# Performance work log

Hardware: AMD Instinct MI355X
Metric: run time of the kernel (lower is better)

## Reference

```python
import jax, jax.numpy as jnp
import numpy as np
from jax import lax

FILTER_SIZE = 3
C_IN = 128
C_OUT = 256
PAD = 1
STRIDE = 1


def setup_inputs() -> dict:
    key = jax.random.key(0)
    k1, k2 = jax.random.split(key)
    prev_a = jax.random.normal(k1, (32, 56, 56, C_IN), dtype=jnp.float32)
    # filter_w initialized ~ N(0, 1) as in the original tf.random.normal
    filter_w = jax.random.normal(k2, (FILTER_SIZE, FILTER_SIZE, C_IN, C_OUT), dtype=jnp.float32)
    filter_b = jnp.zeros((1, 1, 1, C_OUT), dtype=jnp.float32)
    return {"prev_a": prev_a, "filter_w": filter_w, "filter_b": filter_b}


def reference(prev_a, filter_w, filter_b):
    # NHWC input, HWIO filter -> NHWC output; same math as the nested-loop conv:
    # z[i,h,w,c] = sum(prev_a_pad[i, h*s:h*s+f, w*s:w*s+f, :] * W[:,:,:,c]) + b[c]
    z = lax.conv_general_dilated(
        prev_a,
        filter_w,
        window_strides=(STRIDE, STRIDE),
        padding=[(PAD, PAD), (PAD, PAD)],
        dimension_numbers=("NHWC", "HWIO", "NHWC"),
    )
    z = z + filter_b  # bias broadcast over (m, H, W)
    return jax.nn.relu(z)
```

## Files before the change

kernel.cpp:

```cpp
#include <hip/hip_runtime.h>
#include <hip/hip_bf16.h>


#define NIMG 32
#define HH 56
#define WW 56
#define PH 58
#define PW 58
#define CIN 128
#define COUT 256
#define KTOT 1152
#define PAD_ELEMS (NIMG * PH * PW * CIN)

#define BK 32
#define KITERS (KTOT / BK)

typedef __attribute__((ext_vector_type(8))) short bf16x8;
typedef __attribute__((ext_vector_type(4))) short s16x4;
typedef __attribute__((ext_vector_type(4))) float f32x4;

__device__ __forceinline__ short f2bf(float x) {
    union { __hip_bfloat16 b; short s; } u;
    u.b = __float2bfloat16(x);
    return u.s;
}

typedef const void __attribute__((address_space(1)))* gas1_t;
typedef void __attribute__((address_space(3)))* las3_t;
__device__ __forceinline__ void async16(short* lds, const short* g) {
    __builtin_amdgcn_global_load_lds((gas1_t)g, (las3_t)lds, 16, 0, 0);
}

__global__ __launch_bounds__(256) void pack_input(const float* __restrict__ in,
                                                  short* __restrict__ pad) {
    const int tid  = blockIdx.x * 256 + threadIdx.x;
    const int flat = tid * 8;
    const int c8   = flat & (CIN - 1);
    const int rest = flat >> 7;
    const int iw   = rest % PW;
    const int r2   = rest / PW;
    const int ih   = r2 % PH;
    const int img  = r2 / PH;
    bf16x8 v = (bf16x8)0;
    if (ih >= 1 && ih <= HH && iw >= 1 && iw <= WW) {
        const float* p = in + (((size_t)(img * HH + ih - 1) * WW + (iw - 1)) * CIN + c8);
        const float4 x0 = *(const float4*)p;
        const float4 x1 = *(const float4*)(p + 4);
        v.s0 = f2bf(x0.x); v.s1 = f2bf(x0.y); v.s2 = f2bf(x0.z); v.s3 = f2bf(x0.w);
        v.s4 = f2bf(x1.x); v.s5 = f2bf(x1.y); v.s6 = f2bf(x1.z); v.s7 = f2bf(x1.w);
    }
    *(bf16x8*)(pad + flat) = v;
}

__global__ __launch_bounds__(256) void pack_wgt(const float* __restrict__ w,
                                                short* __restrict__ wt) {
    __shared__ short tile[32][33];
    const int k0 = blockIdx.x * 32;
    const int n0 = blockIdx.y * 32;
    const int t  = threadIdx.x;
    {
        const int kl  = t >> 3;
        const int nl4 = (t & 7) * 4;
        const float4 x = *(const float4*)(w + (size_t)(k0 + kl) * COUT + n0 + nl4);
        tile[kl][nl4 + 0] = f2bf(x.x);
        tile[kl][nl4 + 1] = f2bf(x.y);
        tile[kl][nl4 + 2] = f2bf(x.z);
        tile[kl][nl4 + 3] = f2bf(x.w);
    }
    __syncthreads();
    {
        const int nl  = t >> 3;
        const int kl4 = (t & 7) * 4;
        s16x4 v;
        v.x = tile[kl4 + 0][nl];
        v.y = tile[kl4 + 1][nl];
        v.z = tile[kl4 + 2][nl];
        v.w = tile[kl4 + 3][nl];
        *(s16x4*)(wt + (size_t)(n0 + nl) * KTOT + k0 + kl4) = v;
    }
}

__global__ __launch_bounds__(256) void conv_mfma(const short* __restrict__ apad,
                                                 const short* __restrict__ bwt,
                                                 const float* __restrict__ bias,
                                                 float* __restrict__ out) {
    __shared__ short As0[128 * BK], As1[128 * BK];
    __shared__ short Bs0[128 * BK], Bs1[128 * BK];

    const int t  = threadIdx.x;
    const int l  = t & 63;
    const int w  = t >> 6;
    const int m0 = blockIdx.y * 128;
    const int n0 = blockIdx.x * 128;

    const int Lc = (t & 7) ^ ((t >> 3) & 7);
    const int kc = Lc & 3;
    int abase[2], bbase[2];
#pragma unroll
    for (int j = 0; j < 2; ++j) {
        const int r   = 2 * (t >> 3) + (Lc >> 2) + j * 64;
        const int m   = m0 + r;
        const int img = m / (HH * WW);
        const int rem = m - img * (HH * WW);
        const int oh  = rem / WW;
        const int ow  = rem - oh * WW;
        abase[j] = ((img * PH + oh) * PW + ow) * CIN + kc * 8;
        bbase[j] = (n0 + r) * KTOT + kc * 8;
    }

    f32x4 acc[4][4];
#pragma unroll
    for (int i = 0; i < 4; ++i)
#pragma unroll
        for (int j = 0; j < 4; ++j) { f32x4 z = {0.f, 0.f, 0.f, 0.f}; acc[i][j] = z; }

    const int wm = w & 1;
    const int wn = w >> 1;
    const int fr = l & 15;
    const int fq = l >> 4;

#define STAGE(KT, AS, BS) do {                                              \
        const int _fhw  = (KT) >> 2;                                        \
        const int _fh   = _fhw / 3;                                         \
        const int _fw   = _fhw - _fh * 3;                                   \
        const int _aoff = (_fh * PW + _fw) * CIN + ((KT) & 3) * 32;         \
        const int _boff = (KT) * BK;                                        \
        _Pragma("unroll")                                                   \
        for (int _j = 0; _j < 2; ++_j) {                                    \
            async16((AS) + (_j * 256 + w * 64) * 8, apad + abase[_j] + _aoff); \
            async16((BS) + (_j * 256 + w * 64) * 8, bwt + bbase[_j] + _boff); \
        }                                                                   \
    } while (0)

#define FRAG(BASE, R) \
    (*(const bf16x8*)((BASE) + (((R) >> 1) << 6) + \
     (((((R) & 1) << 2) | fq) ^ (((R) >> 1) & 7)) * 8))

#define COMPUTE(AS, BS) do {                                                \
        bf16x8 _af[4], _bf[4];                                              \
        _Pragma("unroll")                                                   \
        for (int _i = 0; _i < 4; ++_i) _af[_i] = FRAG(AS, wm * 64 + _i * 16 + fr); \
        _Pragma("unroll")                                                   \
        for (int _j = 0; _j < 4; ++_j) _bf[_j] = FRAG(BS, wn * 64 + _j * 16 + fr); \
        _Pragma("unroll")                                                   \
        for (int _i = 0; _i < 4; ++_i)                                      \
            _Pragma("unroll")                                               \
            for (int _j = 0; _j < 4; ++_j)                                  \
                acc[_i][_j] = __builtin_amdgcn_mfma_f32_16x16x32_bf16(      \
                    _af[_i], _bf[_j], acc[_i][_j], 0, 0, 0);                \
    } while (0)

    STAGE(0, As0, Bs0);
    for (int kt = 0; kt < KITERS; kt += 2) {
        __syncthreads();
        STAGE(kt + 1, As1, Bs1);
        COMPUTE(As0, Bs0);
        __syncthreads();
        if (kt + 2 < KITERS) STAGE(kt + 2, As0, Bs0);
        COMPUTE(As1, Bs1);
    }

#pragma unroll
    for (int j = 0; j < 4; ++j) {
        const int n  = n0 + wn * 64 + j * 16 + fr;
        const float bj = bias[n];
#pragma unroll
        for (int i = 0; i < 4; ++i) {
            const int mrow = m0 + wm * 64 + i * 16 + fq * 4;
#pragma unroll
            for (int r = 0; r < 4; ++r) {
                const float v = acc[i][j][r] + bj;
                out[(size_t)(mrow + r) * COUT + n] = v > 0.f ? v : 0.f;
            }
        }
    }
#undef STAGE
#undef FRAG
#undef COMPUTE
}

extern "C" void kernel_launch(void* const* d_in, const int* in_sizes, int n_in,
                              void* d_out, int out_size, void* d_ws, size_t ws_size,
                              hipStream_t stream) {
    const float* in   = (const float*)d_in[0];
    const float* wgt  = (const float*)d_in[1];
    const float* bias = (const float*)d_in[2];
    float* out = (float*)d_out;

    short* pad = (short*)d_ws;
    short* wt  = (short*)d_ws + PAD_ELEMS;

    pack_input<<<PAD_ELEMS / 8 / 256, 256, 0, stream>>>(in, pad);
    pack_wgt<<<dim3(KTOT / 32, COUT / 32), 256, 0, stream>>>(wgt, wt);

    dim3 grid(COUT / 128, (NIMG * HH * WW) / 128);
    conv_mfma<<<grid, 256, 0, stream>>>(pad, wt, bias, out);
}
```

Before: 223.2 us.

## Rewrite conv GEMM as 256x256 tile with 8 waves and fine-grained LDS pipeline

The implicit-GEMM conv kernel now uses 512-thread blocks, each covering 256 output pixels across all 256 output channels. K is staged in BK=64 slices split into two 32-wide halves, with double buffering and a multi-phase schedule that interleaves async global-to-LDS loads with MFMA groups. The schedule uses manual s_waitcnt vmcnt and raw barriers, raises wave priority during MFMA bursts, and swizzles block indices for locality. This is meant to raise data reuse per LDS byte and hide load latency. In exchange it needs 128 KB of LDS per block and many more accumulator registers, and the hand-written wait counts are fragile.

Result: faster. 205.0 us (-8.2%).

```diff
diff --git a/kernel.cpp b/kernel.cpp
--- a/kernel.cpp
+++ b/kernel.cpp
@@ -12,8 +12,9 @@
 #define KTOT 1152
 #define PAD_ELEMS (NIMG * PH * PW * CIN)
 
-#define BK 32
-#define KITERS (KTOT / BK)
+#define BK 64
+#define NT (KTOT / BK)
+#define NBLK ((NIMG * HH * WW) / 256)
 
 typedef __attribute__((ext_vector_type(8))) short bf16x8;
 typedef __attribute__((ext_vector_type(4))) short s16x4;
@@ -27,8 +28,8 @@
 
 typedef const void __attribute__((address_space(1)))* gas1_t;
 typedef void __attribute__((address_space(3)))* las3_t;
-__device__ __forceinline__ void async16(short* lds, const short* g) {
-    __builtin_amdgcn_global_load_lds((gas1_t)g, (las3_t)lds, 16, 0, 0);
+__device__ __forceinline__ void async16(short* lds_p, const short* g) {
+    __builtin_amdgcn_global_load_lds((gas1_t)g, (las3_t)lds_p, 16, 0, 0);
 }
 
 __global__ __launch_bounds__(256) void pack_input(const float* __restrict__ in,
@@ -80,103 +81,143 @@
     }
 }
 
-__global__ __launch_bounds__(256) void conv_mfma(const short* __restrict__ apad,
-                                                 const short* __restrict__ bwt,
-                                                 const float* __restrict__ bias,
-                                                 float* __restrict__ out) {
-    __shared__ short As0[128 * BK], As1[128 * BK];
-    __shared__ short Bs0[128 * BK], Bs1[128 * BK];
+#define FENCE() asm volatile("" ::: "memory")
+#define BARRIER() do { FENCE(); __builtin_amdgcn_s_barrier(); FENCE(); } while (0)
+#define VMWAIT(N) asm volatile("s_waitcnt vmcnt(" #N ")" ::: "memory")
+#define NOSTMT ((void)0)
+
+__global__ __launch_bounds__(512, 2) void conv_mfma(const short* __restrict__ apad,
+                                                    const short* __restrict__ bwt,
+                                                    const float* __restrict__ bias,
+                                                    float* __restrict__ out) {
+    __shared__ short lds[65536];
 
     const int t  = threadIdx.x;
     const int l  = t & 63;
     const int w  = t >> 6;
-    const int m0 = blockIdx.y * 128;
-    const int n0 = blockIdx.x * 128;
-
-    const int Lc = (t & 7) ^ ((t >> 3) & 7);
-    const int kc = Lc & 3;
-    int abase[2], bbase[2];
-#pragma unroll
-    for (int j = 0; j < 2; ++j) {
-        const int r   = 2 * (t >> 3) + (Lc >> 2) + j * 64;
-        const int m   = m0 + r;
-        const int img = m / (HH * WW);
-        const int rem = m - img * (HH * WW);
-        const int oh  = rem / WW;
-        const int ow  = rem - oh * WW;
-        abase[j] = ((img * PH + oh) * PW + ow) * CIN + kc * 8;
-        bbase[j] = (n0 + r) * KTOT + kc * 8;
-    }
-
-    f32x4 acc[4][4];
-#pragma unroll
-    for (int i = 0; i < 4; ++i)
-#pragma unroll
-        for (int j = 0; j < 4; ++j) { f32x4 z = {0.f, 0.f, 0.f, 0.f}; acc[i][j] = z; }
-
-    const int wm = w & 1;
-    const int wn = w >> 1;
+    const int wm = w >> 2;
+    const int wn = w & 3;
     const int fr = l & 15;
     const int fq = l >> 4;
 
-#define STAGE(KT, AS, BS) do {                                              \
-        const int _fhw  = (KT) >> 2;                                        \
-        const int _fh   = _fhw / 3;                                         \
-        const int _fw   = _fhw - _fh * 3;                                   \
-        const int _aoff = (_fh * PW + _fw) * CIN + ((KT) & 3) * 32;         \
-        const int _boff = (KT) * BK;                                        \
-        _Pragma("unroll")                                                   \
-        for (int _j = 0; _j < 2; ++_j) {                                    \
-            async16((AS) + (_j * 256 + w * 64) * 8, apad + abase[_j] + _aoff); \
-            async16((BS) + (_j * 256 + w * 64) * 8, bwt + bbase[_j] + _boff); \
-        }                                                                   \
+    const int laneoff = fr * 32 + ((fq ^ ((fr >> 1) & 3))) * 8;
+    const int kcs   = (t & 3) ^ ((t >> 3) & 3);
+    const int wbase = w * 512;
+
+    const int bid = blockIdx.x;
+    const int swz = (bid & 7) * (NBLK / 8) + (bid >> 3);
+    const int m0  = swz * 256;
+
+    const int r0 = t >> 2;
+    int abase0, abase1;
+    {
+        int m = m0 + r0;
+        int img = m / (HH * WW), rem = m - img * (HH * WW);
+        int oh = rem / WW, ow = rem - oh * WW;
+        abase0 = ((img * PH + oh) * PW + ow) * CIN;
+        m = m0 + r0 + 128;
+        img = m / (HH * WW); rem = m - img * (HH * WW);
+        oh = rem / WW; ow = rem - oh * WW;
+        abase1 = ((img * PH + oh) * PW + ow) * CIN;
+    }
+    const int bbase0 = r0 * KTOT;
+    const int bbase1 = (r0 + 128) * KTOT;
+
+    f32x4 acc[8][4];
+#pragma unroll
+    for (int i = 0; i < 8; ++i)
+#pragma unroll
+        for (int j = 0; j < 4; ++j) { f32x4 z = {0.f, 0.f, 0.f, 0.f}; acc[i][j] = z; }
+
+    bf16x8 af[8];
+
+#define STAGE_A(KT, KH) do {                                                  \
+        const int _tap = (KT) >> 1;                                           \
+        const int _fh  = (_tap * 11) >> 5;                   \
+        const int _fw  = _tap - 3 * _fh;                                      \
+        const int _off = (_fh * PW + _fw) * CIN + ((KT) & 1) * 64             \
+                         + (KH) * 32 + kcs * 8;                               \
+        short* _l = lds + (((KT) & 1) * 2 + (KH)) * 8192 + wbase;             \
+        async16(_l,        apad + abase0 + _off);                             \
+        async16(_l + 4096, apad + abase1 + _off);                             \
     } while (0)
 
-#define FRAG(BASE, R) \
-    (*(const bf16x8*)((BASE) + (((R) >> 1) << 6) + \
-     (((((R) & 1) << 2) | fq) ^ (((R) >> 1) & 7)) * 8))
-
-#define COMPUTE(AS, BS) do {                                                \
-        bf16x8 _af[4], _bf[4];                                              \
-        _Pragma("unroll")                                                   \
-        for (int _i = 0; _i < 4; ++_i) _af[_i] = FRAG(AS, wm * 64 + _i * 16 + fr); \
-        _Pragma("unroll")                                                   \
-        for (int _j = 0; _j < 4; ++_j) _bf[_j] = FRAG(BS, wn * 64 + _j * 16 + fr); \
-        _Pragma("unroll")                                                   \
-        for (int _i = 0; _i < 4; ++_i)                                      \
-            _Pragma("unroll")                                               \
-            for (int _j = 0; _j < 4; ++_j)                                  \
-                acc[_i][_j] = __builtin_amdgcn_mfma_f32_16x16x32_bf16(      \
-                    _af[_i], _bf[_j], acc[_i][_j], 0, 0, 0);                \
+#define STAGE_B(KT, KH) do {                                                  \
+        const int _off = (KT) * 64 + (KH) * 32 + kcs * 8;                     \
+        short* _l = lds + 32768 + (((KT) & 1) * 2 + (KH)) * 8192 + wbase;     \
+        async16(_l,        bwt + bbase0 + _off);                              \
+        async16(_l + 4096, bwt + bbase1 + _off);                              \
     } while (0)
 
-    STAGE(0, As0, Bs0);
-    for (int kt = 0; kt < KITERS; kt += 2) {
-        __syncthreads();
-        STAGE(kt + 1, As1, Bs1);
-        COMPUTE(As0, Bs0);
-        __syncthreads();
-        if (kt + 2 < KITERS) STAGE(kt + 2, As0, Bs0);
-        COMPUTE(As1, Bs1);
-    }
+#define PHASE(BUF, KH, NH, STAGE_STMT, WAIT_STMT) do {                        \
+        const short* _a = lds + ((BUF) * 2 + (KH)) * 8192;                    \
+        const short* _b = lds + 32768 + ((BUF) * 2 + (KH)) * 8192;            \
+        bf16x8 _bf0, _bf1;                                                    \
+        if ((NH) == 0) {                                                      \
+            _Pragma("unroll")                                                 \
+            for (int _i = 0; _i < 8; ++_i)                                    \
+                af[_i] = *(const bf16x8*)(_a + wm * 4096 + _i * 512 + laneoff); \
+        }                                                                     \
+        _bf0 = *(const bf16x8*)(_b + wn * 2048 + (NH) * 1024 +   0 + laneoff); \
+        _bf1 = *(const bf16x8*)(_b + wn * 2048 + (NH) * 1024 + 512 + laneoff); \
+        STAGE_STMT;                                                           \
+        BARRIER();                                                            \
+        __builtin_amdgcn_s_setprio(1);                                        \
+        _Pragma("unroll")                                                     \
+        for (int _i = 0; _i < 8; ++_i) {                                      \
+            acc[_i][(NH)*2+0] = __builtin_amdgcn_mfma_f32_16x16x32_bf16(      \
+                af[_i], _bf0, acc[_i][(NH)*2+0], 0, 0, 0);                    \
+            acc[_i][(NH)*2+1] = __builtin_amdgcn_mfma_f32_16x16x32_bf16(      \
+                af[_i], _bf1, acc[_i][(NH)*2+1], 0, 0, 0);                    \
+        }                                                                     \
+        __builtin_amdgcn_s_setprio(0);                                        \
+        WAIT_STMT;                                                            \
+        BARRIER();                                                            \
+    } while (0)
+
+    STAGE_A(0, 0); STAGE_B(0, 0);
+    STAGE_A(0, 1); STAGE_B(0, 1);
+    STAGE_A(1, 0); STAGE_B(1, 0);
+    VMWAIT(8);
+    BARRIER();
+
+#pragma unroll 1
+    for (int kt = 0; kt < NT - 2; kt += 2) {
+        PHASE(0, 0, 0, STAGE_A(kt + 1, 1), NOSTMT);
+        PHASE(0, 0, 1, STAGE_B(kt + 1, 1), VMWAIT(8));
+        PHASE(0, 1, 0, STAGE_A(kt + 2, 0), NOSTMT);
+        PHASE(0, 1, 1, STAGE_B(kt + 2, 0), VMWAIT(8));
+        PHASE(1, 0, 0, STAGE_A(kt + 2, 1), NOSTMT);
+        PHASE(1, 0, 1, STAGE_B(kt + 2, 1), VMWAIT(8));
+        PHASE(1, 1, 0, STAGE_A(kt + 3, 0), NOSTMT);
+        PHASE(1, 1, 1, STAGE_B(kt + 3, 0), VMWAIT(8));
+    }
+    PHASE(0, 0, 0, STAGE_A(NT - 1, 1), NOSTMT);
+    PHASE(0, 0, 1, STAGE_B(NT - 1, 1), VMWAIT(8));
+    PHASE(0, 1, 0, NOSTMT,             NOSTMT);
+    PHASE(0, 1, 1, NOSTMT,             VMWAIT(4));
+    PHASE(1, 0, 0, NOSTMT,             NOSTMT);
+    PHASE(1, 0, 1, NOSTMT,             VMWAIT(0));
+    PHASE(1, 1, 0, NOSTMT,             NOSTMT);
+    PHASE(1, 1, 1, NOSTMT,             NOSTMT);
 
 #pragma unroll
     for (int j = 0; j < 4; ++j) {
-        const int n  = n0 + wn * 64 + j * 16 + fr;
+        const int n  = wn * 64 + j * 16 + fr;
         const float bj = bias[n];
 #pragma unroll
-        for (int i = 0; i < 4; ++i) {
-            const int mrow = m0 + wm * 64 + i * 16 + fq * 4;
+        for (int i = 0; i < 8; ++i) {
+            const int mr = m0 + wm * 128 + i * 16 + fq * 4;
 #pragma unroll
             for (int r = 0; r < 4; ++r) {
                 const float v = acc[i][j][r] + bj;
-                out[(size_t)(mrow + r) * COUT + n] = v > 0.f ? v : 0.f;
+                out[(size_t)(mr + r) * COUT + n] = v > 0.f ? v : 0.f;
             }
         }
     }
-#undef STAGE
-#undef FRAG
-#undef COMPUTE
+#undef STAGE_A
+#undef STAGE_B
+#undef PHASE
 }
 
 extern "C" void kernel_launch(void* const* d_in, const int* in_sizes, int n_in,
@@ -193,6 +234,5 @@
     pack_input<<<PAD_ELEMS / 8 / 256, 256, 0, stream>>>(in, pad);
     pack_wgt<<<dim3(KTOT / 32, COUT / 32), 256, 0, stream>>>(wgt, wt);
 
-    dim3 grid(COUT / 128, (NIMG * HH * WW) / 128);
-    conv_mfma<<<grid, 256, 0, stream>>>(pad, wt, bias, out);
-}
+    conv_mfma<<<NBLK, 512, 0, stream>>>(pad, wt, bias, out);
+}
```
